# Performance work log

Measured on AMD Instinct MI355X. Metric: run time of the kernel, lower is better.

The kernel has to match this reference:

```python
import jax, jax.numpy as jnp
import numpy as np

N_NODES = 100000
N_EDGES = 1600000
D_IN = 128
D_OUT = 128
EPSILON = 0.0


def setup_inputs() -> dict:
    key = jax.random.key(0)
    k1, k2, k3, k4, k5 = jax.random.split(key, 5)
    indices = jax.random.randint(k1, (2, N_EDGES), 0, N_NODES, dtype=jnp.int64 if jax.config.jax_enable_x64 else jnp.int32)
    values = jax.random.uniform(k2, (N_EDGES,), dtype=jnp.float32)
    features = jax.random.normal(k3, (N_NODES, D_IN), dtype=jnp.float32)
    # Xavier-uniform linear weights, zero biases (as in init_parameters)
    lim1 = float(np.sqrt(6.0 / (D_IN + D_OUT)))
    lim2 = float(np.sqrt(6.0 / (D_OUT + D_OUT)))
    W1 = jax.random.uniform(k4, (D_IN, D_OUT), minval=-lim1, maxval=lim1, dtype=jnp.float32)
    W2 = jax.random.uniform(k5, (D_OUT, D_OUT), minval=-lim2, maxval=lim2, dtype=jnp.float32)
    b1 = jnp.zeros((D_OUT,), dtype=jnp.float32)
    b2 = jnp.zeros((D_OUT,), dtype=jnp.float32)
    return {"indices": indices, "values": values, "features": features,
            "W1": W1, "b1": b1, "W2": W2, "b2": b2}


def reference(indices, values, features, W1, b1, W2, b2):
    row, col = indices[0], indices[1]
    # SpMM: out[r] = sum_e values[e] * features[col[e]]  (sparse_adj @ features)
    messages = values[:, None] * features[col]              # [E, D_IN]
    neighbor = jax.ops.segment_sum(messages, row, num_segments=N_NODES)  # [N, D_IN]
    combined = (1.0 + EPSILON) * features + neighbor        # epsilon residual
    h = jax.nn.relu(combined @ W1 + b1)                     # Linear -> ReLU
    out = h @ W2 + b2                                       # Linear
    # dropout is identity in eval mode
    return out
```

## Files before the change

kernel.cpp:

```cpp
#include <hip/hip_runtime.h>

#define N_NODES 100000
#define N_EDGES 1600000
#define D 128
#define NB 782
#define BCAP 2560

typedef unsigned short u16;
typedef unsigned int u32;
typedef __attribute__((ext_vector_type(8))) short bf16x8;
typedef __attribute__((ext_vector_type(4))) float f32x4;

__device__ __forceinline__ u16 f2bf(float f) {
    u32 u = __float_as_uint(f);
    u += 0x7fffu + ((u >> 16) & 1u);
    return (u16)(u >> 16);
}


#define BIN_BLKS 1563
#define CF_BLKS 6250
#define CW_BLKS 128

__global__ __launch_bounds__(256) void prep(
    const float* __restrict__ features, u32* __restrict__ featb,
    const float* __restrict__ W1, const float* __restrict__ W2,
    u16* __restrict__ W1t, u16* __restrict__ W2t,
    const int* __restrict__ row, const int* __restrict__ col,
    const float* __restrict__ val,
    int* __restrict__ bucketCount, int2* __restrict__ binned) {
    __shared__ int hist[NB];
    __shared__ int lbase[NB];
    int bid = blockIdx.x;
    int t = threadIdx.x;

    if (bid >= BIN_BLKS) {
        int cid = bid - BIN_BLKS;
        if (cid < CF_BLKS) {
            int idx = cid * 256 + t;
            const float4* f4 = (const float4*)features;
            float4 a = f4[idx * 2], b = f4[idx * 2 + 1];
            uint4 o;
            o.x = (u32)f2bf(a.x) | ((u32)f2bf(a.y) << 16);
            o.y = (u32)f2bf(a.z) | ((u32)f2bf(a.w) << 16);
            o.z = (u32)f2bf(b.x) | ((u32)f2bf(b.y) << 16);
            o.w = (u32)f2bf(b.z) | ((u32)f2bf(b.w) << 16);
            ((uint4*)featb)[idx] = o;
        } else {
            int flat = (cid - CF_BLKS) * 256 + t;
            int m = flat >> 14;
            int idx = flat & 16383;
            int n = idx & 127;
            int k = idx >> 7;
            const float* src = m ? W2 : W1;
            u16* dst = m ? W2t : W1t;
            dst[n * 128 + k] = f2bf(src[k * 128 + n]);
        }
        return;
    }

    int b = bid;
    for (int i = t; i < NB; i += 256) hist[i] = 0;
    __syncthreads();
    int base = b * 1024;
    int r[4];
#pragma unroll
    for (int i = 0; i < 4; ++i) {
        int e = base + i * 256 + t;
        r[i] = (e < N_EDGES) ? row[e] : -1;
        if (r[i] >= 0) atomicAdd(&hist[r[i] >> 7], 1);
    }
    __syncthreads();
    for (int i = t; i < NB; i += 256) {
        int c = hist[i];
        lbase[i] = c ? atomicAdd(&bucketCount[i], c) : 0;
    }
    __syncthreads();
    for (int i = t; i < NB; i += 256) hist[i] = 0;
    __syncthreads();
#pragma unroll
    for (int i = 0; i < 4; ++i) {
        if (r[i] < 0) continue;
        int e = base + i * 256 + t;
        int bkt = r[i] >> 7;
        int pos = bkt * BCAP + lbase[bkt] + atomicAdd(&hist[bkt], 1);
        int2 ev;
        ev.x = col[e] | ((r[i] & 127) << 17);
        ev.y = __float_as_int(val[e]);
        binned[pos] = ev;
    }
}

__global__ __launch_bounds__(256) void bucket_sort(const int2* __restrict__ binned,
                                                   const int* __restrict__ bucketCount,
                                                   int2* __restrict__ rowRange,
                                                   int2* __restrict__ scev) {
    __shared__ int h[128];
    __shared__ int cur[128];
    __shared__ int2 evs[BCAP];
    int b = blockIdx.x, t = threadIdx.x;
    int row0 = b << 7;
    int nrows = N_NODES - row0;
    if (nrows > 128) nrows = 128;
    if (t < 128) h[t] = 0;
    __syncthreads();
    int lo = b * BCAP;
    int cnt = bucketCount[b];
    for (int i = t; i < cnt; i += 256) {
        int2 ev = binned[lo + i];
        evs[i] = ev;
        atomicAdd(&h[((u32)ev.x) >> 17], 1);
    }
    __syncthreads();
    if (t < 128) cur[t] = h[t];
    __syncthreads();
    for (int d = 1; d < 128; d <<= 1) {
        int x = 0;
        if (t < 128 && t >= d) x = cur[t - d];
        __syncthreads();
        if (t < 128) cur[t] += x;
        __syncthreads();
    }
    if (t < 128) {
        int excl = lo + cur[t] - h[t];
        if (t < nrows) rowRange[row0 + t] = make_int2(excl, excl + h[t]);
        cur[t] = excl;
    }
    __syncthreads();
    for (int i = t; i < cnt; i += 256) {
        int2 ev = evs[i];
        int rl = ((u32)ev.x) >> 17;
        int pos = atomicAdd(&cur[rl], 1);
        scev[pos] = make_int2(ev.x & 0x1FFFF, ev.y);
    }
}


__global__ __launch_bounds__(256) void spmm_bf16(
    const int2* __restrict__ scev, const int2* __restrict__ rowRange,
    const u32* __restrict__ featb, u32* __restrict__ Xb) {
    int wid0 = (blockIdx.x * blockDim.x + threadIdx.x) >> 6;
    int wid = __builtin_amdgcn_readfirstlane(wid0);
    int lane = threadIdx.x & 63;
    if (wid >= N_NODES) return;
    int2 rr = rowRange[wid];
    int j = rr.x, end = rr.y;
    u32 self = featb[wid * 64 + lane];
    float ax0 = __uint_as_float(self << 16);
    float ay0 = __uint_as_float(self & 0xffff0000u);
    float ax1 = 0.f, ay1 = 0.f;
    for (; j < end; j += 16) {
        int2 e[16];
        u32 p[16];
#pragma unroll
        for (int u = 0; u < 16; ++u) {
            int idx = j + u;
            int c = (idx < end) ? idx : (end - 1);
            e[u] = scev[c];
            if (idx >= end) e[u].y = 0;
        }
#pragma unroll
        for (int u = 0; u < 16; ++u) p[u] = featb[e[u].x * 64 + lane];
#pragma unroll
        for (int u = 0; u < 16; ++u) {
            float v = __int_as_float(e[u].y);
            float lo = __uint_as_float(p[u] << 16);
            float hi = __uint_as_float(p[u] & 0xffff0000u);
            if (u & 1) {
                ax1 += v * lo;
                ay1 += v * hi;
            } else {
                ax0 += v * lo;
                ay0 += v * hi;
            }
        }
    }
    float accx = ax0 + ax1;
    float accy = ay0 + ay1;
    Xb[wid * 64 + lane] = (u32)f2bf(accx) | ((u32)f2bf(accy) << 16);
}


__global__ __launch_bounds__(256, 2) void gemm_fused(
    const u16* __restrict__ Xb, const u16* __restrict__ W1t,
    const float* __restrict__ b1, const u16* __restrict__ W2t,
    const float* __restrict__ b2, float* __restrict__ outf) {
    __shared__ u16 Ws[128][136];
    u16(*Ht)[130] = (u16(*)[130]) & Ws[0][0];

    int t = threadIdx.x;
    {
        const uint4* wsrc = (const uint4*)W1t;
#pragma unroll
        for (int i = 0; i < 8; ++i) {
            int f = t + 256 * i;
            *(uint4*)&Ws[f >> 4][(f & 15) << 3] = wsrc[f];
        }
    }
    __syncthreads();

    int w = t >> 6, lane = t & 63;
    int quad = lane >> 4, l16 = lane & 15;
    int row0 = blockIdx.x * 128 + w * 32;

    f32x4 acc[2][8];
#pragma unroll
    for (int rt = 0; rt < 2; ++rt)
#pragma unroll
        for (int ct = 0; ct < 8; ++ct) acc[rt][ct] = (f32x4){0.f, 0.f, 0.f, 0.f};

    int ra = row0 + l16;
    int rb = row0 + 16 + l16;
    if (ra > N_NODES - 1) ra = N_NODES - 1;
    if (rb > N_NODES - 1) rb = N_NODES - 1;
    const u16* pa = Xb + (size_t)ra * D + quad * 8;
    const u16* pb = Xb + (size_t)rb * D + quad * 8;

#pragma unroll
    for (int kb = 0; kb < 128; kb += 32) {
        bf16x8 a0 = *(const bf16x8*)(pa + kb);
        bf16x8 a1 = *(const bf16x8*)(pb + kb);
#pragma unroll
        for (int ct = 0; ct < 8; ++ct) {
            bf16x8 b = *(const bf16x8*)&Ws[ct * 16 + l16][kb + quad * 8];
            acc[0][ct] = __builtin_amdgcn_mfma_f32_16x16x32_bf16(a0, b, acc[0][ct], 0, 0, 0);
            acc[1][ct] = __builtin_amdgcn_mfma_f32_16x16x32_bf16(a1, b, acc[1][ct], 0, 0, 0);
        }
    }

    float bv1[8];
#pragma unroll
    for (int ct = 0; ct < 8; ++ct) bv1[ct] = b1[ct * 16 + l16];

    __syncthreads();

    int hbase = w * 32;
#pragma unroll
    for (int rt = 0; rt < 2; ++rt) {
#pragma unroll
        for (int ct = 0; ct < 8; ++ct) {
            float v0 = fmaxf(acc[rt][ct][0] + bv1[ct], 0.f);
            float v1 = fmaxf(acc[rt][ct][1] + bv1[ct], 0.f);
            float v2 = fmaxf(acc[rt][ct][2] + bv1[ct], 0.f);
            float v3 = fmaxf(acc[rt][ct][3] + bv1[ct], 0.f);
            u16* dst = &Ht[ct * 16 + l16][hbase + rt * 16 + quad * 4];
            ((u32*)dst)[0] = (u32)f2bf(v0) | ((u32)f2bf(v1) << 16);
            ((u32*)dst)[1] = (u32)f2bf(v2) | ((u32)f2bf(v3) << 16);
        }
    }
    __syncthreads();

    f32x4 acc2[2][8];
#pragma unroll
    for (int rt = 0; rt < 2; ++rt)
#pragma unroll
        for (int ct = 0; ct < 8; ++ct) acc2[rt][ct] = (f32x4){0.f, 0.f, 0.f, 0.f};

#pragma unroll
    for (int kb = 0; kb < 128; kb += 32) {
        bf16x8 a0, a1;
#pragma unroll
        for (int i = 0; i < 8; ++i) {
            a0[i] = (short)Ht[kb + quad * 8 + i][hbase + l16];
            a1[i] = (short)Ht[kb + quad * 8 + i][hbase + 16 + l16];
        }
#pragma unroll
        for (int ct = 0; ct < 8; ++ct) {
            bf16x8 b = *(const bf16x8*)(W2t + (size_t)(ct * 16 + l16) * D + kb + quad * 8);
            acc2[0][ct] = __builtin_amdgcn_mfma_f32_16x16x32_bf16(a0, b, acc2[0][ct], 0, 0, 0);
            acc2[1][ct] = __builtin_amdgcn_mfma_f32_16x16x32_bf16(a1, b, acc2[1][ct], 0, 0, 0);
        }
    }

    float bv2[8];
#pragma unroll
    for (int ct = 0; ct < 8; ++ct) bv2[ct] = b2[ct * 16 + l16];

#pragma unroll
    for (int rt = 0; rt < 2; ++rt) {
#pragma unroll
        for (int r = 0; r < 4; ++r) {
            int row = row0 + rt * 16 + quad * 4 + r;
            if (row >= N_NODES) continue;
#pragma unroll
            for (int ct = 0; ct < 8; ++ct) {
                outf[(size_t)row * D + ct * 16 + l16] = acc2[rt][ct][r] + bv2[ct];
            }
        }
    }
}

extern "C" void kernel_launch(void* const* d_in, const int* in_sizes, int n_in,
                              void* d_out, int out_size, void* d_ws, size_t ws_size,
                              hipStream_t stream) {
    const int* indices = (const int*)d_in[0];
    const float* values = (const float*)d_in[1];
    const float* features = (const float*)d_in[2];
    const float* W1 = (const float*)d_in[3];
    const float* b1 = (const float*)d_in[4];
    const float* W2 = (const float*)d_in[5];
    const float* b2 = (const float*)d_in[6];

    const int* row = indices;
    const int* col = indices + N_EDGES;

    int* wsI = (int*)d_ws;
    int* bucketCount = wsI;
    int2* rowRange = (int2*)(wsI + 784);
    int2* scev = (int2*)(wsI + 784 + 2 * N_NODES);
    u32* Xb = (u32*)(wsI + 784 + 2 * N_NODES + 2 * NB * BCAP);
    u16* W1t = (u16*)(Xb + (size_t)N_NODES * 64);
    u16* W2t = W1t + 16384;

    int2* binned = (int2*)d_out;
    u32* featb = (u32*)((char*)d_out + (size_t)N_NODES * D * 2);
    float* outf = (float*)d_out;

    hipMemsetAsync(bucketCount, 0, NB * sizeof(int), stream);

    prep<<<BIN_BLKS + CF_BLKS + CW_BLKS, 256, 0, stream>>>(
        features, featb, W1, W2, W1t, W2t, row, col, values, bucketCount, binned);

    bucket_sort<<<NB, 256, 0, stream>>>(binned, bucketCount, rowRange, scev);

    spmm_bf16<<<(N_NODES * 64 + 255) / 256, 256, 0, stream>>>(scev, rowRange, featb, Xb);

    gemm_fused<<<(N_NODES + 127) / 128, 256, 0, stream>>>(
        (const u16*)Xb, W1t, b1, W2t, b2, outf);
}
```

Measured before the change: 294.2 us.

## Switch edge binning to coarse 1024-row buckets with 1024-thread sort blocks

Edge binning now uses 98 coarse buckets of 1024 rows each instead of 782 buckets of 128 rows. Each binning block handles 4096 edges, and the per-bucket counters are padded 16 ints apart to avoid contention. The second-stage sort runs 98 blocks of 1024 threads, builds the row histogram with wave shuffle scans, and reads binned edges twice from global memory instead of staging them in LDS. The aim is fewer global atomics and fewer, larger blocks, at the cost of only 98 blocks on the sort stage, which may leave much of the GPU idle.

Result: faster. 252.7 us (-14.1%).

```diff
diff --git a/kernel.cpp b/kernel.cpp
--- a/kernel.cpp
+++ b/kernel.cpp
@@ -3,8 +3,8 @@
 #define N_NODES 100000
 #define N_EDGES 1600000
 #define D 128
-#define NB 782
-#define BCAP 2560
+#define CB 98
+#define CCAP 17920
 
 typedef unsigned short u16;
 typedef unsigned int u32;
@@ -18,7 +18,7 @@
 }
 
 
-#define BIN_BLKS 1563
+#define BIN_BLKS 391
 #define CF_BLKS 6250
 #define CW_BLKS 128
 
@@ -28,9 +28,9 @@
     u16* __restrict__ W1t, u16* __restrict__ W2t,
     const int* __restrict__ row, const int* __restrict__ col,
     const float* __restrict__ val,
-    int* __restrict__ bucketCount, int2* __restrict__ binned) {
-    __shared__ int hist[NB];
-    __shared__ int lbase[NB];
+    int* __restrict__ coarseCount, int2* __restrict__ binned) {
+    __shared__ int h[CB];
+    __shared__ int lb[CB];
     int bid = blockIdx.x;
     int t = threadIdx.x;
 
@@ -59,76 +59,83 @@
         return;
     }
 
-    int b = bid;
-    for (int i = t; i < NB; i += 256) hist[i] = 0;
-    __syncthreads();
-    int base = b * 1024;
-    int r[4];
-#pragma unroll
-    for (int i = 0; i < 4; ++i) {
+    if (t < CB) h[t] = 0;
+    __syncthreads();
+    int base = bid * 4096;
+    int r[16];
+#pragma unroll
+    for (int i = 0; i < 16; ++i) {
         int e = base + i * 256 + t;
         r[i] = (e < N_EDGES) ? row[e] : -1;
-        if (r[i] >= 0) atomicAdd(&hist[r[i] >> 7], 1);
-    }
-    __syncthreads();
-    for (int i = t; i < NB; i += 256) {
-        int c = hist[i];
-        lbase[i] = c ? atomicAdd(&bucketCount[i], c) : 0;
-    }
-    __syncthreads();
-    for (int i = t; i < NB; i += 256) hist[i] = 0;
-    __syncthreads();
-#pragma unroll
-    for (int i = 0; i < 4; ++i) {
+        if (r[i] >= 0) atomicAdd(&h[r[i] >> 10], 1);
+    }
+    __syncthreads();
+    if (t < CB) {
+        int c = h[t];
+        lb[t] = c ? atomicAdd(&coarseCount[t * 16], c) : 0;
+        h[t] = 0;
+    }
+    __syncthreads();
+#pragma unroll
+    for (int i = 0; i < 16; ++i) {
         if (r[i] < 0) continue;
         int e = base + i * 256 + t;
-        int bkt = r[i] >> 7;
-        int pos = bkt * BCAP + lbase[bkt] + atomicAdd(&hist[bkt], 1);
+        int cb = r[i] >> 10;
+        int pos = cb * CCAP + lb[cb] + atomicAdd(&h[cb], 1);
         int2 ev;
-        ev.x = col[e] | ((r[i] & 127) << 17);
+        ev.x = col[e] | ((r[i] & 1023) << 17);
         ev.y = __float_as_int(val[e]);
         binned[pos] = ev;
     }
 }
 
-__global__ __launch_bounds__(256) void bucket_sort(const int2* __restrict__ binned,
-                                                   const int* __restrict__ bucketCount,
-                                                   int2* __restrict__ rowRange,
-                                                   int2* __restrict__ scev) {
-    __shared__ int h[128];
-    __shared__ int cur[128];
-    __shared__ int2 evs[BCAP];
+
+__global__ __launch_bounds__(1024) void sortk(const int2* __restrict__ binned,
+                                              const int* __restrict__ coarseCount,
+                                              int2* __restrict__ rowRange,
+                                              int2* __restrict__ scev) {
+    __shared__ int h[1024];
+    __shared__ int cur[1024];
+    __shared__ int wsum[16];
+    __shared__ int wbase[16];
     int b = blockIdx.x, t = threadIdx.x;
-    int row0 = b << 7;
-    int nrows = N_NODES - row0;
-    if (nrows > 128) nrows = 128;
-    if (t < 128) h[t] = 0;
-    __syncthreads();
-    int lo = b * BCAP;
-    int cnt = bucketCount[b];
-    for (int i = t; i < cnt; i += 256) {
+    int lane = t & 63, wv = t >> 6;
+    int row0 = b << 10;
+    int lo = b * CCAP;
+    int cnt = coarseCount[b * 16];
+
+    h[t] = 0;
+    __syncthreads();
+    for (int i = t; i < cnt; i += 1024)
+        atomicAdd(&h[((u32)binned[lo + i].x) >> 17], 1);
+    __syncthreads();
+
+    int c = h[t];
+    int x = c;
+#pragma unroll
+    for (int d = 1; d < 64; d <<= 1) {
+        int y = __shfl_up(x, d);
+        if (lane >= d) x += y;
+    }
+    if (lane == 63) wsum[wv] = x;
+    __syncthreads();
+    if (t < 16) {
+        int s = wsum[t], sx = s;
+#pragma unroll
+        for (int d = 1; d < 16; d <<= 1) {
+            int y = __shfl_up(sx, d);
+            if (lane >= d) sx += y;
+        }
+        wbase[t] = sx - s;
+    }
+    __syncthreads();
+    int start = lo + wbase[wv] + (x - c);
+    if (row0 + t < N_NODES) rowRange[row0 + t] = make_int2(start, start + c);
+    cur[t] = start;
+    __syncthreads();
+
+    for (int i = t; i < cnt; i += 1024) {
         int2 ev = binned[lo + i];
-        evs[i] = ev;
-        atomicAdd(&h[((u32)ev.x) >> 17], 1);
-    }
-    __syncthreads();
-    if (t < 128) cur[t] = h[t];
-    __syncthreads();
-    for (int d = 1; d < 128; d <<= 1) {
-        int x = 0;
-        if (t < 128 && t >= d) x = cur[t - d];
-        __syncthreads();
-        if (t < 128) cur[t] += x;
-        __syncthreads();
-    }
-    if (t < 128) {
-        int excl = lo + cur[t] - h[t];
-        if (t < nrows) rowRange[row0 + t] = make_int2(excl, excl + h[t]);
-        cur[t] = excl;
-    }
-    __syncthreads();
-    for (int i = t; i < cnt; i += 256) {
-        int2 ev = evs[i];
         int rl = ((u32)ev.x) >> 17;
         int pos = atomicAdd(&cur[rl], 1);
         scev[pos] = make_int2(ev.x & 0x1FFFF, ev.y);
@@ -305,10 +312,10 @@
     const int* col = indices + N_EDGES;
 
     int* wsI = (int*)d_ws;
-    int* bucketCount = wsI;
-    int2* rowRange = (int2*)(wsI + 784);
-    int2* scev = (int2*)(wsI + 784 + 2 * N_NODES);
-    u32* Xb = (u32*)(wsI + 784 + 2 * N_NODES + 2 * NB * BCAP);
+    int* coarseCount = wsI;
+    int2* rowRange = (int2*)(wsI + 1600);
+    int2* scev = (int2*)(wsI + 1600 + 2 * N_NODES);
+    u32* Xb = (u32*)(wsI + 1600 + 2 * N_NODES + 2 * CB * CCAP);
     u16* W1t = (u16*)(Xb + (size_t)N_NODES * 64);
     u16* W2t = W1t + 16384;
 
@@ -316,12 +323,12 @@
     u32* featb = (u32*)((char*)d_out + (size_t)N_NODES * D * 2);
     float* outf = (float*)d_out;
 
-    hipMemsetAsync(bucketCount, 0, NB * sizeof(int), stream);
+    hipMemsetAsync(coarseCount, 0, CB * 16 * sizeof(int), stream);
 
     prep<<<BIN_BLKS + CF_BLKS + CW_BLKS, 256, 0, stream>>>(
-        features, featb, W1, W2, W1t, W2t, row, col, values, bucketCount, binned);
-
-    bucket_sort<<<NB, 256, 0, stream>>>(binned, bucketCount, rowRange, scev);
+        features, featb, W1, W2, W1t, W2t, row, col, values, coarseCount, binned);
+
+    sortk<<<CB, 1024, 0, stream>>>(binned, coarseCount, rowRange, scev);
 
     spmm_bf16<<<(N_NODES * 64 + 255) / 256, 256, 0, stream>>>(scev, rowRange, featb, Xb);
 
```
